# Optimization experiments

Measured on AMD Instinct MI355X. Metric: run time of the kernel, lower is better.

Reference implementation:

```python
import jax, jax.numpy as jnp
import numpy as np

W_CUB = 0.1
W_CD = 1.0
W_EXT = 0.01
W_SPS = 0.01
THRED = 24.0
COS_EPS = 1e-4

# cube face buffers (6 faces x 3 coords)
MASK_PROJECT = jnp.array([[0,1,1],[0,1,1],[1,0,1],[1,0,1],[1,1,0],[1,1,0]], jnp.float32)
MASK_PLANE   = jnp.array([[1,0,0],[1,0,0],[0,1,0],[0,1,0],[0,0,1],[0,0,1]], jnp.float32)
CUBE_NORMAL  = jnp.array([[-1,0,0],[1,0,0],[0,-1,0],[0,1,0],[0,0,-1],[0,0,1]], jnp.float32)
# torch repeat(...,3,...) of [[-1,-1,-1],[1,1,1]] tiles it -> [c0,c1,c0,c1,c0,c1]
CUBE_PLANES6 = jnp.tile(jnp.array([[-1.,-1.,-1.],[1.,1.,1.]], jnp.float32), (3,1))


def setup_inputs():
    B, P, N, S = 4, 24, 3072, 128
    key = jax.random.key(0)
    ks = jax.random.split(key, 8)
    pc_inver = jax.random.normal(ks[0], (B, P, N, 3), jnp.float32)
    normals_inver = jax.random.normal(ks[1], (B, P, N, 3), jnp.float32)
    scale = jax.random.uniform(ks[2], (B, P, 3), jnp.float32) * 0.9 + 0.1
    shape = jax.random.uniform(ks[3], (B, P, 2), jnp.float32) * 1.3 + 0.2
    exist = jax.random.uniform(ks[4], (B, P, 1), jnp.float32) * 0.98 + 0.01
    assign_matrix = jax.nn.softmax(jax.random.normal(ks[5], (B, N, P), jnp.float32), axis=-1)
    etas = jax.random.uniform(ks[6], (B, P, S), jnp.float32, minval=-jnp.pi/2, maxval=jnp.pi/2)
    omegas = jax.random.uniform(ks[7], (B, P, S), jnp.float32, minval=-jnp.pi, maxval=jnp.pi)
    return dict(pc_inver=pc_inver, normals_inver=normals_inver, scale=scale,
                shape=shape, exist=exist, assign_matrix=assign_matrix,
                etas=etas, omegas=omegas)


def _fexp(x, p):
    return jnp.sign(x) * jnp.abs(x) ** p


def _sample_sq_points(scale, eps, etas, omegas):
    # scale (B,P,3), eps (B,P,2), etas/omegas (B,P,S) -> (B,P,S,3)
    etas = jnp.where(etas == 0, 1e-6, etas)
    omegas = jnp.where(omegas == 0, 1e-6, omegas)
    a1, a2, a3 = scale[..., 0:1], scale[..., 1:2], scale[..., 2:3]
    e1, e2 = eps[..., 0:1], eps[..., 1:2]
    ce, se = jnp.cos(etas), jnp.sin(etas)
    co, so = jnp.cos(omegas), jnp.sin(omegas)
    x = a1 * _fexp(ce, e1) * _fexp(co, e2)
    y = a2 * _fexp(ce, e1) * _fexp(so, e2)
    z = a3 * _fexp(se, e1)
    fix = lambda v: (jnp.where(v > 0, 1.0, -1.0)) * jnp.maximum(jnp.abs(v), 1e-6)
    return jnp.stack([fix(x), fix(y), fix(z)], -1)


def _cd_loss(pc_inver, scale, shape, exist, assign_matrix, etas, omegas):
    X = _sample_sq_points(scale, shape, etas, omegas)          # (B,P,S,3)
    diff = X[:, :, :, None, :] - pc_inver[:, :, None, :, :]    # (B,P,S,N,3)
    D = jnp.sum(diff * diff, -1)                               # (B,P,S,N)
    pcl2prim = jnp.min(D, axis=2)                              # (B,P,N)
    pcl_loss = jnp.mean(jnp.sum(jnp.swapaxes(pcl2prim, 1, 2) * assign_matrix, -1))
    prim2pcl = jnp.mean(jnp.min(D, axis=3), axis=-1)           # (B,P)
    e = exist[..., 0]
    prim_loss = jnp.mean(jnp.sum(prim2pcl * e, -1) / (jnp.sum(e, -1) + 1e-6))
    return pcl_loss, prim_loss


def _cuboid_loss(pc_inver, normals_inver, scale, assign_matrix):
    pc = jnp.swapaxes(pc_inver, 1, 2)        # (B,N,P,3)
    nrm = jnp.swapaxes(normals_inver, 1, 2)  # (B,N,P,3)
    n_norm = jnp.maximum(jnp.linalg.norm(nrm, axis=-1, keepdims=True), COS_EPS)
    cos = jnp.einsum('bnpc,fc->bnpf', nrm, CUBE_NORMAL) / n_norm  # ||cube_normal||=1
    idx = jnp.argmax(cos, axis=-1)           # (B,N,P)
    s = scale[:, None, :, None, :]           # (B,1,P,1,3)
    proj = pc[:, :, :, None, :] * MASK_PROJECT + (CUBE_PLANES6 * s) * MASK_PLANE  # (B,N,P,6,3)
    proj = jnp.clip(proj, -s, s)
    proj_sel = jnp.take_along_axis(proj, idx[..., None, None], axis=3)[..., 0, :]  # (B,N,P,3)
    d = jnp.sum((proj_sel - pc) ** 2, -1)    # (B,N,P)
    return jnp.mean(jnp.sum(d * assign_matrix, -1))


def _common_losses(assign_matrix, exist):
    gt = jax.lax.stop_gradient((jnp.sum(assign_matrix, 1) > THRED).astype(jnp.float32))  # (B,P)
    p = exist[..., 0]
    bce = -jnp.mean(gt * jnp.log(p) + (1.0 - gt) * jnp.log1p(-p))
    N = assign_matrix.shape[1]
    sps = jnp.mean(jnp.mean(jnp.sqrt(jnp.sum(assign_matrix, 1) / N + 0.01), -1) ** 2)
    return bce, sps


def reference(pc_inver, normals_inver, scale, shape, exist, assign_matrix, etas, omegas):
    cub = _cuboid_loss(pc_inver, normals_inver, scale, assign_matrix)
    pcl_loss, prim_loss = _cd_loss(pc_inver, scale, shape, exist, assign_matrix, etas, omegas)
    bce, sps = _common_losses(assign_matrix, exist)
    return W_CUB * cub + W_CD * (pcl_loss + prim_loss) + W_EXT * bce + W_SPS * sps
```

## Files before the change

### kernel.cpp

```cpp
#include <hip/hip_runtime.h>
#include <math.h>

#define BB 4
#define PP 24
#define NN 3072
#define SS 128
#define CHUNK 512
#define NSPLIT 6
#define PART_STRIDE 132
#define FINF 3.4e38f

__device__ __forceinline__ float fexp_f(float v, float p) {
    float m = powf(fabsf(v), p);
    float s = (v > 0.f) ? 1.f : ((v < 0.f) ? -1.f : 0.f);
    return s * m;
}
__device__ __forceinline__ float fix_f(float v) {
    return ((v > 0.f) ? 1.f : -1.f) * fmaxf(fabsf(v), 1e-6f);
}
__device__ __forceinline__ float wave_sum(float v) {
    #pragma unroll
    for (int off = 32; off > 0; off >>= 1) v += __shfl_down(v, off);
    return v;
}
__device__ __forceinline__ float cub_dist(float px, float py, float pz,
                                          float nx, float ny, float nz,
                                          float sc0, float sc1, float sc2) {
    float best = -nx; int idx = 0;
    if ( nx > best) { best =  nx; idx = 1; }
    if (-ny > best) { best = -ny; idx = 2; }
    if ( ny > best) { best =  ny; idx = 3; }
    if (-nz > best) { best = -nz; idx = 4; }
    if ( nz > best) { best =  nz; idx = 5; }
    const int c = idx >> 1;
    const float scc = (c == 0) ? sc0 : ((c == 1) ? sc1 : sc2);
    const float fv  = (idx & 1) ? scc : -scc;
    float pr0 = (c == 0) ? fv : fminf(fmaxf(px, -sc0), sc0);
    float pr1 = (c == 1) ? fv : fminf(fmaxf(py, -sc1), sc1);
    float pr2 = (c == 2) ? fv : fminf(fmaxf(pz, -sc2), sc2);
    float d0 = pr0 - px, d1 = pr1 - py, d2 = pr2 - pz;
    return fmaf(d0, d0, fmaf(d1, d1, d2 * d2));
}

__global__ __launch_bounds__(256) void superdec_main(
    const float* __restrict__ pc, const float* __restrict__ nrm,
    const float* __restrict__ scale, const float* __restrict__ shape,
    const float* __restrict__ assign,
    const float* __restrict__ etas, const float* __restrict__ omegas,
    float* __restrict__ ws)
{
    const int blk   = blockIdx.x;
    const int bp    = blk / NSPLIT;
    const int split = blk % NSPLIT;
    const int b     = bp / PP;
    const int p     = bp % PP;
    const int tid   = threadIdx.x;
    const int n0    = split * CHUNK;
    const int pid   = tid & 127;
    const int q     = tid >> 7;

    __shared__ float4 Xs[SS];
    __shared__ float4 Pts[CHUNK];
    __shared__ float4 dmin2[2][128];
    __shared__ float  red[8 * SS];
    __shared__ float  wsum[6];

    const float sc0 = scale[bp * 3 + 0];
    const float sc1 = scale[bp * 3 + 1];
    const float sc2 = scale[bp * 3 + 2];

    const float4* pc4 = (const float4*)(pc + ((size_t)bp * NN + n0) * 3);
    const float4 g0 = pc4[pid * 3 + 0];
    const float4 g1 = pc4[pid * 3 + 1];
    const float4 g2 = pc4[pid * 3 + 2];
    const float px0 = g0.x, py0 = g0.y, pz0 = g0.z;
    const float px1 = g0.w, py1 = g1.x, pz1 = g1.y;
    const float px2 = g1.z, py2 = g1.w, pz2 = g2.x;
    const float px3 = g2.y, py3 = g2.z, pz3 = g2.w;
    const float ps0 = fmaf(px0, px0, fmaf(py0, py0, pz0 * pz0));
    const float ps1 = fmaf(px1, px1, fmaf(py1, py1, pz1 * pz1));
    const float ps2 = fmaf(px2, px2, fmaf(py2, py2, pz2 * pz2));
    const float ps3 = fmaf(px3, px3, fmaf(py3, py3, pz3 * pz3));

    float cub0 = 0.f, cub1 = 0.f, cub2 = 0.f, cub3 = 0.f;
    float am0 = 0.f, am1 = 0.f, am2 = 0.f, am3 = 0.f;

    if (q == 0) {
        {
            const float e1 = shape[bp * 2 + 0];
            const float e2 = shape[bp * 2 + 1];
            float eta = etas[bp * SS + tid];
            float omg = omegas[bp * SS + tid];
            eta = (eta == 0.f) ? 1e-6f : eta;
            omg = (omg == 0.f) ? 1e-6f : omg;
            float ce = cosf(eta), se = sinf(eta);
            float co = cosf(omg), so = sinf(omg);
            float fce = fexp_f(ce, e1);
            float x = fix_f(sc0 * fce * fexp_f(co, e2));
            float y = fix_f(sc1 * fce * fexp_f(so, e2));
            float z = fix_f(sc2 * fexp_f(se, e1));
            float xsq = fmaf(x, x, fmaf(y, y, z * z));
            Xs[tid] = make_float4(-2.f * x, -2.f * y, -2.f * z, xsq);
        }
        Pts[pid * 4 + 0] = make_float4(px0, py0, pz0, ps0);
        Pts[pid * 4 + 1] = make_float4(px1, py1, pz1, ps1);
        Pts[pid * 4 + 2] = make_float4(px2, py2, pz2, ps2);
        Pts[pid * 4 + 3] = make_float4(px3, py3, pz3, ps3);
        const float4* nr4 = (const float4*)(nrm + ((size_t)bp * NN + n0) * 3);
        const float4 h0 = nr4[pid * 3 + 0];
        const float4 h1 = nr4[pid * 3 + 1];
        const float4 h2 = nr4[pid * 3 + 2];
        cub0 = cub_dist(px0, py0, pz0, h0.x, h0.y, h0.z, sc0, sc1, sc2);
        cub1 = cub_dist(px1, py1, pz1, h0.w, h1.x, h1.y, sc0, sc1, sc2);
        cub2 = cub_dist(px2, py2, pz2, h1.z, h1.w, h2.x, sc0, sc1, sc2);
        cub3 = cub_dist(px3, py3, pz3, h2.y, h2.z, h2.w, sc0, sc1, sc2);
        const size_t abase = ((size_t)b * NN + n0 + pid * 4) * PP + p;
        am0 = assign[abase + 0 * PP];
        am1 = assign[abase + 1 * PP];
        am2 = assign[abase + 2 * PP];
        am3 = assign[abase + 3 * PP];
    }
    __syncthreads();

    {
        const int sb = q * 64;
        float m0 = FINF, m1 = FINF, m2 = FINF, m3 = FINF;
        #pragma unroll 4
        for (int s = 0; s < 64; s += 2) {
            float4 xa = Xs[sb + s];
            float4 xb = Xs[sb + s + 1];
            float d;
            d = fmaf(xa.x, px0, fmaf(xa.y, py0, fmaf(xa.z, pz0, xa.w))); m0 = fminf(m0, d);
            d = fmaf(xa.x, px1, fmaf(xa.y, py1, fmaf(xa.z, pz1, xa.w))); m1 = fminf(m1, d);
            d = fmaf(xa.x, px2, fmaf(xa.y, py2, fmaf(xa.z, pz2, xa.w))); m2 = fminf(m2, d);
            d = fmaf(xa.x, px3, fmaf(xa.y, py3, fmaf(xa.z, pz3, xa.w))); m3 = fminf(m3, d);
            d = fmaf(xb.x, px0, fmaf(xb.y, py0, fmaf(xb.z, pz0, xb.w))); m0 = fminf(m0, d);
            d = fmaf(xb.x, px1, fmaf(xb.y, py1, fmaf(xb.z, pz1, xb.w))); m1 = fminf(m1, d);
            d = fmaf(xb.x, px2, fmaf(xb.y, py2, fmaf(xb.z, pz2, xb.w))); m2 = fminf(m2, d);
            d = fmaf(xb.x, px3, fmaf(xb.y, py3, fmaf(xb.z, pz3, xb.w))); m3 = fminf(m3, d);
        }
        dmin2[q][pid] = make_float4(m0, m1, m2, m3);
    }
    __syncthreads();

    if (q == 0) {
        float4 a = dmin2[0][pid];
        float4 c = dmin2[1][pid];
        float d0 = fminf(a.x, c.x) + ps0;
        float d1 = fminf(a.y, c.y) + ps1;
        float d2 = fminf(a.z, c.z) + ps2;
        float d3 = fminf(a.w, c.w) + ps3;
        float acc_pcl = d0 * am0 + d1 * am1 + d2 * am2 + d3 * am3;
        float acc_cub = cub0 * am0 + cub1 * am1 + cub2 * am2 + cub3 * am3;
        float acc_am  = am0 + am1 + am2 + am3;
        float s0 = wave_sum(acc_pcl);
        float s1 = wave_sum(acc_cub);
        float s2 = wave_sum(acc_am);
        const int lane = tid & 63, wave = tid >> 6;
        if (lane == 0) {
            wsum[wave * 3 + 0] = s0;
            wsum[wave * 3 + 1] = s1;
            wsum[wave * 3 + 2] = s2;
        }
    }

    {
        const int rep = tid >> 5;
        const int sb  = tid & 31;
        const float4 x0 = Xs[sb];
        const float4 x1 = Xs[sb + 32];
        const float4 x2 = Xs[sb + 64];
        const float4 x3 = Xs[sb + 96];
        const int nb = rep * 64;
        float r0 = FINF, r1 = FINF, r2 = FINF, r3 = FINF;
        #pragma unroll 4
        for (int n = 0; n < 64; n += 2) {
            float4 pa = Pts[nb + n];
            float4 pb = Pts[nb + n + 1];
            float d;
            d = fmaf(x0.x, pa.x, fmaf(x0.y, pa.y, fmaf(x0.z, pa.z, pa.w))); r0 = fminf(r0, d);
            d = fmaf(x1.x, pa.x, fmaf(x1.y, pa.y, fmaf(x1.z, pa.z, pa.w))); r1 = fminf(r1, d);
            d = fmaf(x2.x, pa.x, fmaf(x2.y, pa.y, fmaf(x2.z, pa.z, pa.w))); r2 = fminf(r2, d);
            d = fmaf(x3.x, pa.x, fmaf(x3.y, pa.y, fmaf(x3.z, pa.z, pa.w))); r3 = fminf(r3, d);
            d = fmaf(x0.x, pb.x, fmaf(x0.y, pb.y, fmaf(x0.z, pb.z, pb.w))); r0 = fminf(r0, d);
            d = fmaf(x1.x, pb.x, fmaf(x1.y, pb.y, fmaf(x1.z, pb.z, pb.w))); r1 = fminf(r1, d);
            d = fmaf(x2.x, pb.x, fmaf(x2.y, pb.y, fmaf(x2.z, pb.z, pb.w))); r2 = fminf(r2, d);
            d = fmaf(x3.x, pb.x, fmaf(x3.y, pb.y, fmaf(x3.z, pb.z, pb.w))); r3 = fminf(r3, d);
        }
        red[rep * SS + sb +  0] = r0;
        red[rep * SS + sb + 32] = r1;
        red[rep * SS + sb + 64] = r2;
        red[rep * SS + sb + 96] = r3;
    }
    __syncthreads();

    float* part = ws + (size_t)(bp * NSPLIT + split) * PART_STRIDE;
    if (tid < SS) {
        float m = red[tid];
        #pragma unroll
        for (int r = 1; r < 8; ++r) m = fminf(m, red[r * SS + tid]);
        part[tid] = m + Xs[tid].w;
    }
    if (tid == 0) {
        part[SS + 0] = wsum[0] + wsum[3];
        part[SS + 1] = wsum[1] + wsum[4];
        part[SS + 2] = wsum[2] + wsum[5];
    }
}

__global__ __launch_bounds__(1024) void superdec_reduce_final(
    const float* __restrict__ ws, const float* __restrict__ exist,
    float* __restrict__ out)
{
    __shared__ float s_prim[96];
    __shared__ float s_pcl[96], s_cub[96], s_bce[96], s_e[96], s_sq[96];
    const int t    = threadIdx.x;
    const int lane = t & 63;
    if (t < 96) s_prim[t] = 0.f;
    __syncthreads();

    #pragma unroll
    for (int k = 0; k < (96 * 128) / 1024; ++k) {
        const int idx = t + k * 1024;
        const int bp  = idx >> 7;
        const int s   = idx & 127;
        const float* base = ws + (size_t)bp * (NSPLIT * PART_STRIDE) + s;
        float m = fminf(fminf(fminf(base[0 * PART_STRIDE], base[1 * PART_STRIDE]),
                              fminf(base[2 * PART_STRIDE], base[3 * PART_STRIDE])),
                        fminf(base[4 * PART_STRIDE], base[5 * PART_STRIDE]));
        float sm = wave_sum(m);
        if (lane == 0) atomicAdd(&s_prim[bp], sm);
    }

    if (t < 96) {
        const float* base = ws + (size_t)t * (NSPLIT * PART_STRIDE) + SS;
        float pcl = 0.f, cub = 0.f, cs = 0.f;
        #pragma unroll
        for (int sp = 0; sp < NSPLIT; ++sp) {
            pcl += base[sp * PART_STRIDE + 0];
            cub += base[sp * PART_STRIDE + 1];
            cs  += base[sp * PART_STRIDE + 2];
        }
        const float e  = exist[t];
        const float gt = (cs > 24.0f) ? 1.f : 0.f;
        s_pcl[t] = pcl;
        s_cub[t] = cub;
        s_bce[t] = gt * logf(e) + (1.f - gt) * log1pf(-e);
        s_e[t]   = e;
        s_sq[t]  = sqrtf(cs / (float)NN + 0.01f);
    }
    __syncthreads();

    if (t == 0) {
        float pcl_sum = 0.f, cub_sum = 0.f, bce_sum = 0.f, prim_loss = 0.f, sps = 0.f;
        #pragma unroll
        for (int b_ = 0; b_ < BB; ++b_) {
            float pe = 0.f, ee = 0.f, sq = 0.f;
            #pragma unroll
            for (int p_ = 0; p_ < PP; ++p_) {
                const int i = b_ * PP + p_;
                pcl_sum += s_pcl[i];
                cub_sum += s_cub[i];
                bce_sum += s_bce[i];
                pe += (s_prim[i] / (float)SS) * s_e[i];
                ee += s_e[i];
                sq += s_sq[i];
            }
            prim_loss += pe / (ee + 1e-6f);
            float mb = sq / (float)PP;
            sps += mb * mb;
        }
        prim_loss /= (float)BB;
        sps       /= (float)BB;
        float pcl_loss = pcl_sum / (float)(BB * NN);
        float cub      = cub_sum / (float)(BB * NN);
        float bce      = -bce_sum / (float)(BB * PP);
        out[0] = 0.1f * cub + 1.0f * (pcl_loss + prim_loss) + 0.01f * bce + 0.01f * sps;
    }
}

extern "C" void kernel_launch(void* const* d_in, const int* in_sizes, int n_in,
                              void* d_out, int out_size, void* d_ws, size_t ws_size,
                              hipStream_t stream) {
    const float* pc     = (const float*)d_in[0];
    const float* nrm    = (const float*)d_in[1];
    const float* scale  = (const float*)d_in[2];
    const float* shape  = (const float*)d_in[3];
    const float* exist  = (const float*)d_in[4];
    const float* assign = (const float*)d_in[5];
    const float* etas   = (const float*)d_in[6];
    const float* omegas = (const float*)d_in[7];
    float* ws  = (float*)d_ws;
    float* out = (float*)d_out;

    superdec_main<<<BB * PP * NSPLIT, 256, 0, stream>>>(
        pc, nrm, scale, shape, assign, etas, omegas, ws);
    superdec_reduce_final<<<1, 1024, 0, stream>>>(ws, exist, out);
}
```

Measured before the change: 94.43 us.

## Fuse final reduction into main kernel via atomics and last-block detection

After: 114.0 us. +20.8%, slower.

```diff
diff --git a/kernel.cpp b/kernel.cpp
--- a/kernel.cpp
+++ b/kernel.cpp
@@ -7,8 +7,12 @@
 #define SS 128
 #define CHUNK 512
 #define NSPLIT 6
-#define PART_STRIDE 132
+#define NBLK (BB * PP * NSPLIT)
 #define FINF 3.4e38f
+
+#define WS_MIN  0
+#define WS_SUM  12288
+#define WS_CNT  12576
 
 __device__ __forceinline__ float fexp_f(float v, float p) {
     float m = powf(fabsf(v), p);
@@ -22,6 +26,9 @@
     #pragma unroll
     for (int off = 32; off > 0; off >>= 1) v += __shfl_down(v, off);
     return v;
+}
+__device__ __forceinline__ float agent_load(const float* p) {
+    return __hip_atomic_load(p, __ATOMIC_RELAXED, __HIP_MEMORY_SCOPE_AGENT);
 }
 __device__ __forceinline__ float cub_dist(float px, float py, float pz,
                                           float nx, float ny, float nz,
@@ -47,7 +54,8 @@
     const float* __restrict__ scale, const float* __restrict__ shape,
     const float* __restrict__ assign,
     const float* __restrict__ etas, const float* __restrict__ omegas,
-    float* __restrict__ ws)
+    const float* __restrict__ exist,
+    float* __restrict__ ws, float* __restrict__ out)
 {
     const int blk   = blockIdx.x;
     const int bp    = blk / NSPLIT;
@@ -64,6 +72,8 @@
     __shared__ float4 dmin2[2][128];
     __shared__ float  red[8 * SS];
     __shared__ float  wsum[6];
+    __shared__ int    s_last;
+    __shared__ float s_prim[96], s_pcl[96], s_cub[96], s_bce[96], s_e[96], s_sq[96];
 
     const float sc0 = scale[bp * 3 + 0];
     const float sc1 = scale[bp * 3 + 1];
@@ -194,64 +204,54 @@
     }
     __syncthreads();
 
-    float* part = ws + (size_t)(bp * NSPLIT + split) * PART_STRIDE;
     if (tid < SS) {
         float m = red[tid];
         #pragma unroll
         for (int r = 1; r < 8; ++r) m = fminf(m, red[r * SS + tid]);
-        part[tid] = m + Xs[tid].w;
+        m = fmaxf(m + Xs[tid].w, 0.f);
+        atomicMin((int*)(ws + WS_MIN + bp * SS + tid), __float_as_int(m));
     }
     if (tid == 0) {
-        part[SS + 0] = wsum[0] + wsum[3];
-        part[SS + 1] = wsum[1] + wsum[4];
-        part[SS + 2] = wsum[2] + wsum[5];
-    }
-}
-
-__global__ __launch_bounds__(1024) void superdec_reduce_final(
-    const float* __restrict__ ws, const float* __restrict__ exist,
-    float* __restrict__ out)
-{
-    __shared__ float s_prim[96];
-    __shared__ float s_pcl[96], s_cub[96], s_bce[96], s_e[96], s_sq[96];
-    const int t    = threadIdx.x;
-    const int lane = t & 63;
-    if (t < 96) s_prim[t] = 0.f;
+        atomicAdd(ws + WS_SUM + bp * 3 + 0, wsum[0] + wsum[3]);
+        atomicAdd(ws + WS_SUM + bp * 3 + 1, wsum[1] + wsum[4]);
+        atomicAdd(ws + WS_SUM + bp * 3 + 2, wsum[2] + wsum[5]);
+    }
+    __syncthreads();
+    if (tid == 0) {
+        int old = atomicAdd((int*)(ws + WS_CNT), 1);
+        s_last = (old == NBLK - 1) ? 1 : 0;
+    }
+    __syncthreads();
+    if (!s_last) return;
+
+    const int lane = tid & 63;
+    if (tid < 96) s_prim[tid] = 0.f;
     __syncthreads();
 
     #pragma unroll
-    for (int k = 0; k < (96 * 128) / 1024; ++k) {
-        const int idx = t + k * 1024;
-        const int bp  = idx >> 7;
-        const int s   = idx & 127;
-        const float* base = ws + (size_t)bp * (NSPLIT * PART_STRIDE) + s;
-        float m = fminf(fminf(fminf(base[0 * PART_STRIDE], base[1 * PART_STRIDE]),
-                              fminf(base[2 * PART_STRIDE], base[3 * PART_STRIDE])),
-                        fminf(base[4 * PART_STRIDE], base[5 * PART_STRIDE]));
+    for (int k = 0; k < (96 * SS) / 256; ++k) {
+        const int idx = tid + k * 256;
+        const int bpi = idx >> 7;
+        float m = agent_load(ws + WS_MIN + idx);
         float sm = wave_sum(m);
-        if (lane == 0) atomicAdd(&s_prim[bp], sm);
-    }
-
-    if (t < 96) {
-        const float* base = ws + (size_t)t * (NSPLIT * PART_STRIDE) + SS;
-        float pcl = 0.f, cub = 0.f, cs = 0.f;
-        #pragma unroll
-        for (int sp = 0; sp < NSPLIT; ++sp) {
-            pcl += base[sp * PART_STRIDE + 0];
-            cub += base[sp * PART_STRIDE + 1];
-            cs  += base[sp * PART_STRIDE + 2];
-        }
-        const float e  = exist[t];
-        const float gt = (cs > 24.0f) ? 1.f : 0.f;
-        s_pcl[t] = pcl;
-        s_cub[t] = cub;
-        s_bce[t] = gt * logf(e) + (1.f - gt) * log1pf(-e);
-        s_e[t]   = e;
-        s_sq[t]  = sqrtf(cs / (float)NN + 0.01f);
-    }
-    __syncthreads();
-
-    if (t == 0) {
+        if (lane == 0) atomicAdd(&s_prim[bpi], sm);
+    }
+
+    if (tid < 96) {
+        const float pcl = agent_load(ws + WS_SUM + tid * 3 + 0);
+        const float cb  = agent_load(ws + WS_SUM + tid * 3 + 1);
+        const float cs  = agent_load(ws + WS_SUM + tid * 3 + 2);
+        const float e   = exist[tid];
+        const float gt  = (cs > 24.0f) ? 1.f : 0.f;
+        s_pcl[tid] = pcl;
+        s_cub[tid] = cb;
+        s_bce[tid] = gt * logf(e) + (1.f - gt) * log1pf(-e);
+        s_e[tid]   = e;
+        s_sq[tid]  = sqrtf(cs / (float)NN + 0.01f);
+    }
+    __syncthreads();
+
+    if (tid == 0) {
         float pcl_sum = 0.f, cub_sum = 0.f, bce_sum = 0.f, prim_loss = 0.f, sps = 0.f;
         #pragma unroll
         for (int b_ = 0; b_ < BB; ++b_) {
@@ -273,9 +273,9 @@
         prim_loss /= (float)BB;
         sps       /= (float)BB;
         float pcl_loss = pcl_sum / (float)(BB * NN);
-        float cub      = cub_sum / (float)(BB * NN);
+        float cubL     = cub_sum / (float)(BB * NN);
         float bce      = -bce_sum / (float)(BB * PP);
-        out[0] = 0.1f * cub + 1.0f * (pcl_loss + prim_loss) + 0.01f * bce + 0.01f * sps;
+        out[0] = 0.1f * cubL + 1.0f * (pcl_loss + prim_loss) + 0.01f * bce + 0.01f * sps;
     }
 }
 
@@ -293,7 +293,9 @@
     float* ws  = (float*)d_ws;
     float* out = (float*)d_out;
 
-    superdec_main<<<BB * PP * NSPLIT, 256, 0, stream>>>(
-        pc, nrm, scale, shape, assign, etas, omegas, ws);
-    superdec_reduce_final<<<1, 1024, 0, stream>>>(ws, exist, out);
-}
+    hipMemsetAsync(ws + WS_MIN, 0x7f, (size_t)(96 * SS) * sizeof(float), stream);
+    hipMemsetAsync(ws + WS_SUM, 0, (size_t)(96 * 3 + 1) * sizeof(float), stream);
+
+    superdec_main<<<NBLK, 256, 0, stream>>>(
+        pc, nrm, scale, shape, assign, etas, omegas, exist, ws, out);
+}
```
